# Performance work log

Hardware: AMD Instinct MI355X
Metric: run time of the kernel (lower is better)

The kernel has to match this reference:

```python
import jax, jax.numpy as jnp
import numpy as np

EPS_BN = 1e-5      # torch BatchNorm2d default eps
EPSILON = 1e-12    # signed-sqrt eps from the module
K = 3              # hardcoded k in forward


def _knn_idx(f, k):
    # f: [B, C, N] -> idx [B, N, k] of nearest neighbors (largest -dist^2)
    xx = jnp.sum(f * f, axis=1)                      # [B, N]
    inner = jnp.einsum('bcn,bcm->bnm', f, f)         # [B, N, N]
    pd = -xx[:, :, None] + 2.0 * inner - xx[:, None, :]
    return jax.lax.top_k(pd, k)[1]                   # [B, N, k]


def _graph_feature(f, k):
    # f: [B, C, N] -> [B, N, k, 2C] = concat(neighbor - center, center)
    idx = _knn_idx(f, k)
    ft = jnp.transpose(f, (0, 2, 1))                 # [B, N, C]
    neigh = jax.vmap(lambda x, i: x[i])(ft, idx)     # [B, N, k, C]
    center = jnp.broadcast_to(ft[:, :, None, :], neigh.shape)
    return jnp.concatenate([neigh - center, center], axis=-1)


def _edgeconv(f, W, gamma, beta, mean, var, k):
    # f: [B, C, N]; W: [O, 2C] (1x1 conv, no bias); eval-mode BN; LeakyReLU(0.2); max over k
    g = _graph_feature(f, k)                         # [B, N, k, 2C]
    y = jnp.einsum('bnkc,oc->bonk', g, W)            # [B, O, N, k]
    scale = (gamma / jnp.sqrt(var + EPS_BN))[None, :, None, None]
    y = (y - mean[None, :, None, None]) * scale + beta[None, :, None, None]
    y = jnp.where(y >= 0, y, 0.2 * y)                # LeakyReLU(0.2)
    return jnp.max(y, axis=-1)                       # [B, O, N]


def setup_inputs() -> dict:
    key = jax.random.key(0)
    ks = jax.random.split(key, 12)
    B, C, H, W, M = 64, 768, 26, 26, 32
    inp = {
        'features': jax.random.normal(ks[0], (B, C, H, W), jnp.float32),
        'attentions': jax.random.uniform(ks[1], (B, M, H, W), jnp.float32),
        'W1': jax.random.normal(ks[2], (C, 2 * C), jnp.float32) * 0.02,
        'gamma1': jax.random.uniform(ks[3], (C,), jnp.float32, 0.5, 1.5),
        'beta1': jax.random.normal(ks[4], (C,), jnp.float32) * 0.1,
        'mean1': jax.random.normal(ks[5], (C,), jnp.float32) * 0.1,
        'var1': jax.random.uniform(ks[6], (C,), jnp.float32, 0.5, 1.5),
        'W2': jax.random.normal(ks[7], (C, 2 * C), jnp.float32) * 0.02,
        'gamma2': jax.random.uniform(ks[8], (C,), jnp.float32, 0.5, 1.5),
        'beta2': jax.random.normal(ks[9], (C,), jnp.float32) * 0.1,
        'mean2': jax.random.normal(ks[10], (C,), jnp.float32) * 0.1,
        'var2': jax.random.uniform(ks[11], (C,), jnp.float32, 0.5, 1.5),
    }
    return inp


def reference(features, attentions, W1, gamma1, beta1, mean1, var1,
              W2, gamma2, beta2, mean2, var2):
    B = features.shape[0]
    # AdaptiveMaxPool2d(1) of features * attn_m, per attention map m.
    # lax.map over M avoids materializing the [B, M, C, H, W] product.
    def per_m(attn_m):                                # attn_m: [B, H, W]
        return jnp.max(features * attn_m[:, None, :, :], axis=(2, 3))  # [B, C]
    fm = jax.lax.map(per_m, jnp.transpose(attentions, (1, 0, 2, 3)))   # [M, B, C]
    fm = jnp.transpose(fm, (1, 2, 0))                 # [B, C, M]

    f1 = _edgeconv(fm, W1, gamma1, beta1, mean1, var1, K)   # [B, C, M]
    f2 = _edgeconv(f1, W2, gamma2, beta2, mean2, var2, K)   # [B, C, M]

    fuse = jnp.concatenate([f1, f2], axis=1).reshape(B, -1)  # [B, 2C*M]
    fuse = jnp.sign(fuse) * jnp.sqrt(jnp.abs(fuse) + EPSILON)
    norm = jnp.maximum(jnp.linalg.norm(fuse, axis=-1, keepdims=True), 1e-12)
    return fuse / norm
```

## Files before the change

### kernel.cpp

```cpp
#include <hip/hip_runtime.h>
#include <cfloat>
#include <cmath>

#define B_    64
#define C_    768
#define HW_   676
#define M_    32
#define TWOC_ 1536

__global__ __launch_bounds__(256) void pool_kernel(
    const float* __restrict__ feat, const float* __restrict__ attn,
    float* __restrict__ fm)
{
    const int b      = blockIdx.x / 12;
    const int cchunk = blockIdx.x % 12;
    const int t  = threadIdx.x;
    const int cl = t >> 2;
    const int m0 = (t & 3) * 8;
    const int c  = cchunk * 64 + cl;

    __shared__ float a_s[64][32];

    float acc[8];
#pragma unroll
    for (int j = 0; j < 8; ++j) acc[j] = -FLT_MAX;

    const float* fp = feat + ((size_t)b * C_ + c) * HW_;
    const float* ap = attn + (size_t)b * M_ * HW_;

    for (int hw0 = 0; hw0 < HW_; hw0 += 64) {
        const int hwlen = min(64, HW_ - hw0);
        __syncthreads();
        for (int idx = t; idx < 64 * 32; idx += 256) {
            int hw = idx >> 5, m = idx & 31;
            if (hw < hwlen) a_s[hw][m] = ap[m * HW_ + hw0 + hw];
        }
        __syncthreads();
        for (int hw = 0; hw < hwlen; hw += 4) {
            float4 f4 = *(const float4*)(fp + hw0 + hw);
            float fv[4] = {f4.x, f4.y, f4.z, f4.w};
#pragma unroll
            for (int q = 0; q < 4; ++q) {
                float f = fv[q];
#pragma unroll
                for (int j = 0; j < 8; ++j) {
                    float p = __fmul_rn(f, a_s[hw + q][m0 + j]);
                    acc[j] = fmaxf(acc[j], p);
                }
            }
        }
    }
    float* op = fm + ((size_t)b * C_ + c) * M_ + m0;
#pragma unroll
    for (int j = 0; j < 8; ++j) op[j] = acc[j];
}

__global__ __launch_bounds__(1024) void knn_kernel(
    const float* __restrict__ X, int* __restrict__ idxout)
{
    const int b = blockIdx.x;
    const int t = threadIdx.x;
    const int n = t >> 5, m = t & 31;

    __shared__ float xs[96][32];
    __shared__ float GF[32][32];
    __shared__ float G2[32][32];
    __shared__ float XS[32];
    __shared__ float XP[32];
    __shared__ float PA[32][32], PC[32][32], PDm[32][32];

    const float* Xb = X + (size_t)b * (C_ * M_);
    float accF = 0.f;
    float accP0 = 0.f, accP1 = 0.f;
    float accXs = 0.f;
    float leaf[8];

#pragma unroll
    for (int chunk = 0; chunk < 8; ++chunk) {
        __syncthreads();
        for (int i = t; i < 96 * 32; i += 1024)
            xs[i >> 5][i & 31] = Xb[(size_t)(chunk * 96 + (i >> 5)) * M_ + (i & 31)];
        __syncthreads();
#pragma unroll
        for (int c = 0; c < 96; ++c)
            accF = __fmaf_rn(xs[c][n], xs[c][m], accF);
        if (chunk < 4) {
#pragma unroll
            for (int c = 0; c < 96; ++c)
                accP0 = __fmaf_rn(xs[c][n], xs[c][m], accP0);
        } else {
#pragma unroll
            for (int c = 0; c < 96; ++c)
                accP1 = __fmaf_rn(xs[c][n], xs[c][m], accP1);
        }
        if (t < 32) {
#pragma unroll
            for (int c = 0; c < 96; ++c) {
                float v = xs[c][m];
                accXs = __fadd_rn(accXs, __fmul_rn(v, v));
            }
            float r[8];
#pragma unroll
            for (int j = 0; j < 8; ++j) {
                float v = xs[j][m];
                r[j] = __fmul_rn(v, v);
            }
            for (int i = 8; i < 96; i += 8) {
#pragma unroll
                for (int j = 0; j < 8; ++j) {
                    float v = xs[i + j][m];
                    r[j] = __fadd_rn(r[j], __fmul_rn(v, v));
                }
            }
            leaf[chunk] = __fadd_rn(
                __fadd_rn(__fadd_rn(r[0], r[1]), __fadd_rn(r[2], r[3])),
                __fadd_rn(__fadd_rn(r[4], r[5]), __fadd_rn(r[6], r[7])));
        }
    }
    GF[n][m] = accF;
    G2[n][m] = __fadd_rn(accP0, accP1);
    if (t < 32) {
        XS[m] = accXs;
        XP[m] = __fadd_rn(
            __fadd_rn(__fadd_rn(leaf[0], leaf[1]), __fadd_rn(leaf[2], leaf[3])),
            __fadd_rn(__fadd_rn(leaf[4], leaf[5]), __fadd_rn(leaf[6], leaf[7])));
    }
    __syncthreads();
    PA[n][m]  = __fsub_rn(__fadd_rn(-XS[n], 2.0f * GF[n][m]), XS[m]);
    PC[n][m]  = __fsub_rn(__fadd_rn(-XP[n], 2.0f * G2[n][m]), XP[m]);
    PDm[n][m] = __fsub_rn(__fadd_rn(-XP[n], 2.0f * GF[n][m]), XP[m]);
    __syncthreads();

    if (t < 32) {
        const int nn = t;
        const float* pa = PA[nn];
        const float* pc = PC[nn];
        const float* pd = PDm[nn];

        unsigned masks[3] = {0u, 0u, 0u};
        const float* rows[3] = {pa, pc, pd};
#pragma unroll
        for (int s = 0; s < 3; ++s) {
            unsigned chosen = 0;
            for (int p = 0; p < 3; ++p) {
                float best = -FLT_MAX; int bi = 0;
                for (int mm = 0; mm < 32; ++mm) {
                    if (chosen & (1u << mm)) continue;
                    float v = rows[s][mm];
                    if (v > best) { best = v; bi = mm; }
                }
                chosen |= 1u << bi;
            }
            masks[s] = chosen;
        }
        const unsigned mA = masks[0], mC = masks[1], mD = masks[2];

        unsigned chosen = 0;
        for (int p = 0; p < 3; ++p) {
            int bv = -1; float bp = -FLT_MAX; int bi = 0;
            for (int mm = 0; mm < 32; ++mm) {
                if (chosen & (1u << mm)) continue;
                int v = (int)((mA >> mm) & 1u) + (int)((mC >> mm) & 1u)
                      + (int)((mD >> mm) & 1u);
                float q = pd[mm];
                if (v > bv || (v == bv && q > bp)) { bv = v; bp = q; bi = mm; }
            }
            chosen |= 1u << bi;
            idxout[((size_t)b * 32 + nn) * 3 + p] = bi;
        }
    }
}

__global__ __launch_bounds__(1024, 4) void conv_kernel(
    const float* __restrict__ X, const float* __restrict__ W,
    const int* __restrict__ idx,
    const float* __restrict__ gamma, const float* __restrict__ beta,
    const float* __restrict__ mean,  const float* __restrict__ var,
    float* __restrict__ fout)
{
    const int b  = blockIdx.x / 12;
    const int oT = blockIdx.x % 12;
    const int o0 = oT * 64;
    const int t  = threadIdx.x;
    const int oG = t >> 4;
    const int nkg = t & 15;

    __shared__ float fs[C_ * M_];
    __shared__ int   idx_s[M_ * 3];

    const float* Xb = X + (size_t)b * (C_ * M_);
    for (int i = t; i < (C_ * M_) / 4; i += 1024)
        ((float4*)fs)[i] = ((const float4*)Xb)[i];
    if (t < 96) idx_s[t] = idx[b * 96 + t];
    __syncthreads();

    const int n_0 = nkg * 2;
    int nn_[6], jj[6];
#pragma unroll
    for (int q = 0; q < 6; ++q) {
        nn_[q] = n_0 + (q >= 3 ? 1 : 0);
        jj[q]  = idx_s[nn_[q] * 3 + (q % 3)];
    }

    const int o = o0 + oG;
    const float* Wr = W + (size_t)o * TWOC_;

    float A[6], Bv[6], Cv[6], Dv[6];

    auto sweep = [&](int lane, float (&OUT)[6]) {
#pragma unroll
        for (int q = 0; q < 6; ++q) OUT[q] = 0.f;
        for (int c = lane; c < C_; c += 8) {
            float w = Wr[c];
#pragma unroll
            for (int q = 0; q < 6; ++q) {
                float g = __fsub_rn(fs[c * 32 + jj[q]], fs[c * 32 + nn_[q]]);
                OUT[q] = __fmaf_rn(w, g, OUT[q]);
            }
        }
        for (int c = C_ + lane; c < TWOC_; c += 8) {
            float w = Wr[c];
#pragma unroll
            for (int q = 0; q < 6; ++q) {
                float g = fs[(c - C_) * 32 + nn_[q]];
                OUT[q] = __fmaf_rn(w, g, OUT[q]);
            }
        }
    };
    auto add6 = [&](float (&Xa)[6], float (&Ya)[6]) {
#pragma unroll
        for (int q = 0; q < 6; ++q)
            Xa[q] = __fadd_rn(Xa[q], Ya[q]);
    };

    sweep(0, A);  sweep(4, Bv); add6(A, Bv);
    sweep(2, Bv); sweep(6, Cv); add6(Bv, Cv);
    add6(A, Bv);
    sweep(1, Bv); sweep(5, Cv); add6(Bv, Cv);
    sweep(3, Cv); sweep(7, Dv); add6(Cv, Dv);
    add6(Bv, Cv);
    add6(A, Bv);

    const float sc = __fdiv_rn(gamma[o], __fsqrt_rn(__fadd_rn(var[o], 1e-5f)));
    const float mu = mean[o], be = beta[o];
#pragma unroll
    for (int nl = 0; nl < 2; ++nl) {
        float r = -FLT_MAX;
#pragma unroll
        for (int k = 0; k < 3; ++k) {
            float y = A[nl * 3 + k];
            y = __fadd_rn(__fmul_rn(__fsub_rn(y, mu), sc), be);
            y = (y >= 0.f) ? y : __fmul_rn(0.2f, y);
            r = fmaxf(r, y);
        }
        fout[((size_t)b * C_ + o) * M_ + (n_0 + nl)] = r;
    }
}

__global__ __launch_bounds__(256) void fuse_kernel(
    const float* __restrict__ f1, const float* __restrict__ f2,
    float* __restrict__ out)
{
    const int b = blockIdx.x;
    const int t = threadIdx.x;
    const float* p1 = f1 + (size_t)b * (C_ * M_);
    const float* p2 = f2 + (size_t)b * (C_ * M_);
    float* po = out + (size_t)b * (2 * C_ * M_);

    __shared__ double red[256];

    double lsum = 0.0;
    for (int i = t; i < 2 * C_ * M_; i += 256) {
        float x = (i < C_ * M_) ? p1[i] : p2[i - C_ * M_];
        float sq = __fsqrt_rn(__fadd_rn(fabsf(x), 1e-12f));
        float s = (x > 0.f) ? sq : ((x < 0.f) ? -sq : 0.f);
        lsum += (double)s * (double)s;
    }
    red[t] = lsum;
    __syncthreads();
    for (int off = 128; off > 0; off >>= 1) {
        if (t < off) red[t] += red[t + off];
        __syncthreads();
    }
    const float normf = fmaxf((float)sqrt(red[0]), 1e-12f);
    for (int i = t; i < 2 * C_ * M_; i += 256) {
        float x = (i < C_ * M_) ? p1[i] : p2[i - C_ * M_];
        float sq = __fsqrt_rn(__fadd_rn(fabsf(x), 1e-12f));
        float s = (x > 0.f) ? sq : ((x < 0.f) ? -sq : 0.f);
        po[i] = __fdiv_rn(s, normf);
    }
}

extern "C" void kernel_launch(void* const* d_in, const int* in_sizes, int n_in,
                              void* d_out, int out_size, void* d_ws, size_t ws_size,
                              hipStream_t stream)
{
    const float* feat = (const float*)d_in[0];
    const float* attn = (const float*)d_in[1];
    const float* W1   = (const float*)d_in[2];
    const float* g1   = (const float*)d_in[3];
    const float* be1  = (const float*)d_in[4];
    const float* mu1  = (const float*)d_in[5];
    const float* va1  = (const float*)d_in[6];
    const float* W2   = (const float*)d_in[7];
    const float* g2   = (const float*)d_in[8];
    const float* be2  = (const float*)d_in[9];
    const float* mu2  = (const float*)d_in[10];
    const float* va2  = (const float*)d_in[11];

    const size_t FM = (size_t)B_ * C_ * M_;
    float* fm  = (float*)d_ws;
    float* f1  = fm + FM;
    float* f2  = f1 + FM;
    int* idx1  = (int*)(f2 + FM);
    int* idx2  = idx1 + B_ * M_ * 3;

    pool_kernel<<<dim3(768), dim3(256), 0, stream>>>(feat, attn, fm);
    knn_kernel<<<dim3(64), dim3(1024), 0, stream>>>(fm, idx1);
    conv_kernel<<<dim3(768), dim3(1024), 0, stream>>>(fm, W1, idx1, g1, be1, mu1, va1, f1);
    knn_kernel<<<dim3(64), dim3(1024), 0, stream>>>(f1, idx2);
    conv_kernel<<<dim3(768), dim3(1024), 0, stream>>>(f1, W2, idx2, g2, be2, mu2, va2, f2);
    fuse_kernel<<<dim3(64), dim3(256), 0, stream>>>(f1, f2, (float*)d_out);
}
```

Baseline: 1.374 ms.

## Restructure edgeconv conv kernel as shared-memory tiled GEMM with register blocking

The conv kernel no longer stages the whole per-batch feature matrix in shared memory with one output row per thread group. It now loops over 64-wide channel tiles, gathers the edge features (neighbor minus center, or center) into a shared tile, stages the weight tile, and computes a 4x6 register-blocked outer product per thread with 256-thread blocks. This is meant to increase data reuse of weights and gathered features and cut the redundant per-thread gather arithmetic and weight reloads from global memory. In exchange it adds extra synchronisation per tile and changes the floating-point summation order relative to the previous carefully ordered reduction.

```diff
diff --git a/kernel.cpp b/kernel.cpp
--- a/kernel.cpp
+++ b/kernel.cpp
@@ -171,7 +171,7 @@
     }
 }
 
-__global__ __launch_bounds__(1024, 4) void conv_kernel(
+__global__ __launch_bounds__(256) void conv_kernel(
     const float* __restrict__ X, const float* __restrict__ W,
     const int* __restrict__ idx,
     const float* __restrict__ gamma, const float* __restrict__ beta,
@@ -182,78 +182,90 @@
     const int oT = blockIdx.x % 12;
     const int o0 = oT * 64;
     const int t  = threadIdx.x;
-    const int oG = t >> 4;
-    const int nkg = t & 15;
-
-    __shared__ float fs[C_ * M_];
-    __shared__ int   idx_s[M_ * 3];
+    const int tx = t & 15;
+    const int ty = t >> 4;
+
+    __shared__ float fs_t[64][33];
+    __shared__ float g_s[96][68];
+    __shared__ float w_s[64][68];
+    __shared__ int   idx_s[96];
+
+    if (t < 96) idx_s[t] = idx[b * 96 + t];
+
+    float acc[4][6] = {};
 
     const float* Xb = X + (size_t)b * (C_ * M_);
-    for (int i = t; i < (C_ * M_) / 4; i += 1024)
-        ((float4*)fs)[i] = ((const float4*)Xb)[i];
-    if (t < 96) idx_s[t] = idx[b * 96 + t];
-    __syncthreads();
-
-    const int n_0 = nkg * 2;
-    int nn_[6], jj[6];
-#pragma unroll
-    for (int q = 0; q < 6; ++q) {
-        nn_[q] = n_0 + (q >= 3 ? 1 : 0);
-        jj[q]  = idx_s[nn_[q] * 3 + (q % 3)];
-    }
-
-    const int o = o0 + oG;
-    const float* Wr = W + (size_t)o * TWOC_;
-
-    float A[6], Bv[6], Cv[6], Dv[6];
-
-    auto sweep = [&](int lane, float (&OUT)[6]) {
-#pragma unroll
-        for (int q = 0; q < 6; ++q) OUT[q] = 0.f;
-        for (int c = lane; c < C_; c += 8) {
-            float w = Wr[c];
-#pragma unroll
-            for (int q = 0; q < 6; ++q) {
-                float g = __fsub_rn(fs[c * 32 + jj[q]], fs[c * 32 + nn_[q]]);
-                OUT[q] = __fmaf_rn(w, g, OUT[q]);
-            }
-        }
-        for (int c = C_ + lane; c < TWOC_; c += 8) {
-            float w = Wr[c];
-#pragma unroll
-            for (int q = 0; q < 6; ++q) {
-                float g = fs[(c - C_) * 32 + nn_[q]];
-                OUT[q] = __fmaf_rn(w, g, OUT[q]);
-            }
-        }
-    };
-    auto add6 = [&](float (&Xa)[6], float (&Ya)[6]) {
-#pragma unroll
-        for (int q = 0; q < 6; ++q)
-            Xa[q] = __fadd_rn(Xa[q], Ya[q]);
-    };
-
-    sweep(0, A);  sweep(4, Bv); add6(A, Bv);
-    sweep(2, Bv); sweep(6, Cv); add6(Bv, Cv);
-    add6(A, Bv);
-    sweep(1, Bv); sweep(5, Cv); add6(Bv, Cv);
-    sweep(3, Cv); sweep(7, Dv); add6(Cv, Dv);
-    add6(Bv, Cv);
-    add6(A, Bv);
-
-    const float sc = __fdiv_rn(gamma[o], __fsqrt_rn(__fadd_rn(var[o], 1e-5f)));
-    const float mu = mean[o], be = beta[o];
-#pragma unroll
-    for (int nl = 0; nl < 2; ++nl) {
-        float r = -FLT_MAX;
-#pragma unroll
-        for (int k = 0; k < 3; ++k) {
-            float y = A[nl * 3 + k];
-            y = __fadd_rn(__fmul_rn(__fsub_rn(y, mu), sc), be);
-            y = (y >= 0.f) ? y : __fmul_rn(0.2f, y);
-            r = fmaxf(r, y);
-        }
-        fout[((size_t)b * C_ + o) * M_ + (n_0 + nl)] = r;
+
+    for (int ct = 0; ct < 24; ++ct) {
+        const int c0 = ct * 64;
+        const bool diff = (c0 < C_);
+        const int crow0 = diff ? c0 : (c0 - C_);
+        __syncthreads();
+        for (int e = t; e < 512; e += 256) {
+            int cl = e >> 3, mq = (e & 7) * 4;
+            float4 v = *(const float4*)(Xb + (size_t)(crow0 + cl) * M_ + mq);
+            fs_t[cl][mq + 0] = v.x; fs_t[cl][mq + 1] = v.y;
+            fs_t[cl][mq + 2] = v.z; fs_t[cl][mq + 3] = v.w;
+        }
+        for (int e = t; e < 1024; e += 256) {
+            int o = e >> 4, cq = (e & 15) * 4;
+            float4 v = *(const float4*)(W + (size_t)(o0 + o) * TWOC_ + c0 + cq);
+            *(float4*)&w_s[o][cq] = v;
+        }
+        __syncthreads();
+        for (int e = t; e < 96 * 64; e += 256) {
+            int s = e >> 6, cl = e & 63;
+            int n = s & 31, k = s >> 5;
+            float v;
+            if (diff) {
+                int j = idx_s[n * 3 + k];
+                v = __fsub_rn(fs_t[cl][j], fs_t[cl][n]);
+            } else {
+                v = fs_t[cl][n];
+            }
+            g_s[s][cl] = v;
+        }
+        __syncthreads();
+        for (int c4 = 0; c4 < 64; c4 += 4) {
+            float4 wv[4], gv[6];
+#pragma unroll
+            for (int i = 0; i < 4; ++i)
+                wv[i] = *(const float4*)&w_s[ty * 4 + i][c4];
+#pragma unroll
+            for (int q = 0; q < 6; ++q)
+                gv[q] = *(const float4*)&g_s[tx + 16 * q][c4];
+#pragma unroll
+            for (int i = 0; i < 4; ++i)
+#pragma unroll
+                for (int q = 0; q < 6; ++q) {
+                    float a = acc[i][q];
+                    a = __fmaf_rn(wv[i].x, gv[q].x, a);
+                    a = __fmaf_rn(wv[i].y, gv[q].y, a);
+                    a = __fmaf_rn(wv[i].z, gv[q].z, a);
+                    a = __fmaf_rn(wv[i].w, gv[q].w, a);
+                    acc[i][q] = a;
+                }
+        }
+    }
+
+#pragma unroll
+    for (int i = 0; i < 4; ++i) {
+        const int o = o0 + ty * 4 + i;
+        const float sc = __fdiv_rn(gamma[o], __fsqrt_rn(__fadd_rn(var[o], 1e-5f)));
+        const float mu = mean[o], be = beta[o];
+#pragma unroll
+        for (int half = 0; half < 2; ++half) {
+            const int n = tx + 16 * half;
+            float r = -FLT_MAX;
+#pragma unroll
+            for (int k = 0; k < 3; ++k) {
+                float y = acc[i][2 * k + half];
+                y = __fadd_rn(__fmul_rn(__fsub_rn(y, mu), sc), be);
+                y = (y >= 0.f) ? y : __fmul_rn(0.2f, y);
+                r = fmaxf(r, y);
+            }
+            fout[((size_t)b * C_ + o) * M_ + n] = r;
+        }
     }
 }
 
@@ -317,8 +329,8 @@
 
     pool_kernel<<<dim3(768), dim3(256), 0, stream>>>(feat, attn, fm);
     knn_kernel<<<dim3(64), dim3(1024), 0, stream>>>(fm, idx1);
-    conv_kernel<<<dim3(768), dim3(1024), 0, stream>>>(fm, W1, idx1, g1, be1, mu1, va1, f1);
+    conv_kernel<<<dim3(768), dim3(256), 0, stream>>>(fm, W1, idx1, g1, be1, mu1, va1, f1);
     knn_kernel<<<dim3(64), dim3(1024), 0, stream>>>(f1, idx2);
-    conv_kernel<<<dim3(768), dim3(1024), 0, stream>>>(f1, W2, idx2, g2, be2, mu2, va2, f2);
+    conv_kernel<<<dim3(768), dim3(256), 0, stream>>>(f1, W2, idx2, g2, be2, mu2, va2, f2);
     fuse_kernel<<<dim3(64), dim3(256), 0, stream>>>(f1, f2, (float*)d_out);
 }
```

Result: faster. 1.120 ms (-18.5%).
